# Performance work log

Hardware: AMD Instinct MI355X
Metric: run time of the kernel (lower is better)

## Reference

```python
import jax, jax.numpy as jnp
import numpy as np

N_NODES = 20000
N_EDGES = 320000
IN_F = 256
OUT_F = 64
HEADS = 4
ALPHA = 0.1  # leaky_relu negative slope


def setup_inputs() -> dict:
    key = jax.random.key(0)
    ks = jax.random.split(key, 8)
    return {
        "input1": jax.random.normal(ks[0], (N_NODES, IN_F), jnp.float32),
        "input2": jax.random.normal(ks[1], (N_NODES, IN_F), jnp.float32),
        # per-head params: Ws maps source feats -> target_out, Wt maps target feats -> source_out
        "Ws": jax.random.normal(ks[2], (HEADS, IN_F, OUT_F), jnp.float32) * 0.06,
        "Wt": jax.random.normal(ks[3], (HEADS, IN_F, OUT_F), jnp.float32) * 0.06,
        "a1": jax.random.normal(ks[4], (HEADS, 2 * OUT_F), jnp.float32) * 0.1,
        "a2": jax.random.normal(ks[5], (HEADS, 2 * OUT_F), jnp.float32) * 0.1,
        # COO nonzeros of A_opt [n_target, n_source]
        "tgt_idx": jax.random.randint(ks[6], (N_EDGES,), 0, N_NODES),
        "src_idx": jax.random.randint(ks[7], (N_EDGES,), 0, N_NODES),
    }


def _segment_softmax(scores, seg, num_segments):
    m = jax.lax.stop_gradient(jax.ops.segment_max(scores, seg, num_segments=num_segments))
    w = jnp.exp(scores - m[seg])
    d = jax.ops.segment_sum(w, seg, num_segments=num_segments)
    d = jnp.where(d == 0, 1.0, d)
    return w / d[seg]


def _head(x1, x2, Ws, Wt, a1, a2, src, tgt, n_s, n_t):
    s = x1 @ Ws  # [n_s, OUT_F]  messages source -> target
    t = x2 @ Wt  # [n_t, OUT_F]  messages target -> source
    out = Ws.shape[1]
    # edge score e = leaky_relu(a^T [s_src || t_tgt]); split a to avoid edge-level concat
    e1 = jax.nn.leaky_relu((s @ a1[:out])[src] + (t @ a1[out:])[tgt], ALPHA)
    e2 = jax.nn.leaky_relu((s @ a2[:out])[src] + (t @ a2[out:])[tgt], ALPHA)
    alpha_ts = _segment_softmax(e1, tgt, n_t)  # softmax over sources per target
    alpha_st = _segment_softmax(e2, src, n_s)  # softmax over targets per source
    h_ts = jax.ops.segment_sum(alpha_ts[:, None] * s[src], tgt, num_segments=n_t)
    h_st = jax.ops.segment_sum(alpha_st[:, None] * t[tgt], src, num_segments=n_s)
    return jax.nn.elu(h_st), jax.nn.elu(h_ts)  # concat=True -> ELU per head


def reference(input1, input2, Ws, Wt, a1, a2, tgt_idx, src_idx):
    n_s, n_t = input1.shape[0], input2.shape[0]
    head_fn = jax.vmap(
        lambda W1, W2, v1, v2: _head(input1, input2, W1, W2, v1, v2, src_idx, tgt_idx, n_s, n_t)
    )
    h_st, h_ts = head_fn(Ws, Wt, a1, a2)  # each [H, n, OUT_F]
    h_st = jnp.transpose(h_st, (1, 0, 2)).reshape(n_s, -1)  # concat heads
    h_ts = jnp.transpose(h_ts, (1, 0, 2)).reshape(n_t, -1)
    return h_st, h_ts
```

## Files before the change

### kernel.cpp

```cpp
#include <hip/hip_runtime.h>
#include <math.h>

#define N_NODES 20000
#define N_EDGES 320000
#define IN_F 256
#define OUT_F 64
#define HEADS 4
#define NCOL 256
#define LRELU_ALPHA 0.1f
#define ELL_CAP 64

typedef __attribute__((ext_vector_type(8))) short short8;
typedef __attribute__((ext_vector_type(4))) float floatx4;

__device__ __forceinline__ float lrelu(float x) {
    return x > 0.f ? x : LRELU_ALPHA * x;
}
__device__ __forceinline__ unsigned short f2bf(float f) {
    unsigned int u = __float_as_uint(f);
    u = (u + 0x7FFF + ((u >> 16) & 1)) >> 16;
    return (unsigned short)u;
}
__device__ __forceinline__ float bf2f(unsigned short u) {
    return __uint_as_float(((unsigned int)u) << 16);
}

__global__ __launch_bounds__(256) void prep_w_kernel(
    const float* __restrict__ Ws, const float* __restrict__ Wt,
    unsigned short* __restrict__ Wsb, unsigned short* __restrict__ Wtb,
    int* __restrict__ cnt)
{
    const int gid = blockIdx.x * 256 + threadIdx.x;

    for (int i = gid; i < 2 * N_NODES; i += 16384) cnt[i] = 0;

    const int mat = gid >> 13;
    const int r   = gid & 8191;
    const int kc  = r >> 8;
    const int c   = r & 255;
    const float* W    = mat ? Wt : Ws;
    unsigned short* O = mat ? Wtb : Wsb;
    const int h = c >> 6, j = c & 63;
    const int k0 = kc * 8;
    unsigned short v[8] __attribute__((aligned(16)));
#pragma unroll
    for (int i = 0; i < 8; ++i)
        v[i] = f2bf(W[(size_t)h * (IN_F * OUT_F) + (size_t)(k0 + i) * OUT_F + j]);
    *(uint4*)(O + (size_t)c * IN_F + k0) = *(const uint4*)v;
}

__global__ __launch_bounds__(256) void gemm_mfma_kernel(
    const float* __restrict__ A0, const unsigned short* __restrict__ Wb0,
    const float* __restrict__ A1, const unsigned short* __restrict__ Wb1,
    unsigned short* __restrict__ C0, unsigned short* __restrict__ C1,
    const float* __restrict__ a1, const float* __restrict__ a2,
    float* __restrict__ ss1, float* __restrict__ ss2,
    float* __restrict__ tt1, float* __restrict__ tt2,
    const int* __restrict__ src, const int* __restrict__ tgt,
    int* __restrict__ cnt_t, int* __restrict__ cnt_s,
    int* __restrict__ elist_t, int* __restrict__ elist_s)
{
    const int tid = threadIdx.x;

    {
        const int e = (blockIdx.y * 625 + blockIdx.x) * 256 + tid;
        int sn = src[e], tn = tgt[e];
        int p = atomicAdd(&cnt_t[tn], 1);
        if (p < ELL_CAP) elist_t[tn * ELL_CAP + p] = sn;
        int q = atomicAdd(&cnt_s[sn], 1);
        if (q < ELL_CAP) elist_s[sn * ELL_CAP + q] = tn;
    }

    const float* A           = (blockIdx.y == 0) ? A0 : A1;
    const unsigned short* Wb = (blockIdx.y == 0) ? Wb0 : Wb1;
    unsigned short* C        = (blockIdx.y == 0) ? C0 : C1;

    __shared__ __align__(16) unsigned short Bl[256][40];

    const int lane  = tid & 63;
    const int w     = tid >> 6;
    const int quad  = lane >> 4;
    const int l15   = lane & 15;
    const int mhalf = w & 1, nhalf = w >> 1;
    const int r0    = blockIdx.x * 32;
    const int mrow  = r0 + mhalf * 16 + l15;

    floatx4 acc[8];
#pragma unroll
    for (int t = 0; t < 8; ++t) acc[t] = (floatx4){0.f, 0.f, 0.f, 0.f};

    const float* arow = A + (size_t)mrow * IN_F + quad * 8;

    for (int k0 = 0; k0 < IN_F; k0 += 32) {
#pragma unroll
        for (int p = 0; p < 4; ++p) {
            int idx = p * 256 + tid;
            int n = idx >> 2, kc = idx & 3;
            uint4 v = *(const uint4*)(Wb + (size_t)n * 256 + k0 + kc * 8);
            *(uint4*)&Bl[n][kc * 8] = v;
        }
        __syncthreads();

        float4 av0 = *(const float4*)(arow + k0);
        float4 av1 = *(const float4*)(arow + k0 + 4);
        short8 afrag;
        afrag[0] = (short)f2bf(av0.x); afrag[1] = (short)f2bf(av0.y);
        afrag[2] = (short)f2bf(av0.z); afrag[3] = (short)f2bf(av0.w);
        afrag[4] = (short)f2bf(av1.x); afrag[5] = (short)f2bf(av1.y);
        afrag[6] = (short)f2bf(av1.z); afrag[7] = (short)f2bf(av1.w);

#pragma unroll
        for (int t = 0; t < 8; ++t) {
            int n = (nhalf * 8 + t) * 16 + l15;
            short8 bfrag = *(const short8*)&Bl[n][quad * 8];
            acc[t] = __builtin_amdgcn_mfma_f32_16x16x32_bf16(afrag, bfrag, acc[t], 0, 0, 0);
        }
        __syncthreads();
    }

#pragma unroll
    for (int t = 0; t < 8; ++t) {
        int col = (nhalf * 8 + t) * 16 + l15;
#pragma unroll
        for (int r = 0; r < 4; ++r) {
            int m = r0 + mhalf * 16 + quad * 4 + r;
            C[(size_t)m * NCOL + col] = f2bf(acc[t][r]);
        }
    }

    const int off_aj = (blockIdx.y == 0) ? 0 : 64;
    float* o1 = (blockIdx.y == 0) ? ss1 : tt1;
    float* o2 = (blockIdx.y == 0) ? ss2 : tt2;

    float p1[2][4] = {{0.f,0.f,0.f,0.f},{0.f,0.f,0.f,0.f}};
    float p2[2][4] = {{0.f,0.f,0.f,0.f},{0.f,0.f,0.f,0.f}};
#pragma unroll
    for (int t = 0; t < 8; ++t) {
        int hh = 2 * nhalf + (t >> 2);
        int jj = ((t & 3) * 16) + l15;
        float w1 = a1[hh * 128 + off_aj + jj];
        float w2 = a2[hh * 128 + off_aj + jj];
        int a = t >> 2;
#pragma unroll
        for (int r = 0; r < 4; ++r) {
            p1[a][r] += acc[t][r] * w1;
            p2[a][r] += acc[t][r] * w2;
        }
    }
#pragma unroll
    for (int m = 1; m < 16; m <<= 1) {
#pragma unroll
        for (int a = 0; a < 2; ++a)
#pragma unroll
            for (int r = 0; r < 4; ++r) {
                p1[a][r] += __shfl_xor(p1[a][r], m, 64);
                p2[a][r] += __shfl_xor(p2[a][r], m, 64);
            }
    }
    if (l15 == 0) {
#pragma unroll
        for (int r = 0; r < 4; ++r) {
            int m = r0 + mhalf * 16 + quad * 4 + r;
#pragma unroll
            for (int a = 0; a < 2; ++a) {
                int hh = 2 * nhalf + a;
                o1[m * HEADS + hh] = p1[a][r];
                o2[m * HEADS + hh] = p2[a][r];
            }
        }
    }
}

__global__ __launch_bounds__(256) void agg_kernel(
    const int* __restrict__ cnt_t, const int* __restrict__ elist_t,
    const int* __restrict__ cnt_s, const int* __restrict__ elist_s,
    const float* __restrict__ ss1, const float* __restrict__ ss2,
    const float* __restrict__ tt1, const float* __restrict__ tt2,
    const unsigned short* __restrict__ s_bf, const unsigned short* __restrict__ t_bf,
    float* __restrict__ h_st, float* __restrict__ h_ts)
{
    const int wave = threadIdx.x >> 6;
    const int lane = threadIdx.x & 63;
    const int n    = blockIdx.x * 4 + wave;
    const int dir  = blockIdx.y;
    const int h    = lane >> 4;
    const int coff = lane * 4;

    const int*            cnt   = dir ? cnt_s   : cnt_t;
    const int*            list  = dir ? elist_s : elist_t;
    const unsigned short* table = dir ? t_bf    : s_bf;
    const float*          nsc   = dir ? ss2     : tt1;
    const float*          esc   = dir ? tt2     : ss1;
    float*                outp  = dir ? h_st    : h_ts;

    const float base = nsc[n * HEADS + h];
    int deg = cnt[n];
    if (deg > ELL_CAP) deg = ELL_CAP;
    const int b0 = n * ELL_CAP, b1 = b0 + deg;

    float4 acc = make_float4(0.f, 0.f, 0.f, 0.f);
    float den = 0.f;

    int p = b0;
    for (; p + 3 < b1; p += 4) {
        int m0 = list[p],     m1 = list[p + 1];
        int m2 = list[p + 2], m3 = list[p + 3];
        float e0 = esc[m0 * HEADS + h], e1 = esc[m1 * HEADS + h];
        float e2 = esc[m2 * HEADS + h], e3 = esc[m3 * HEADS + h];
        ushort4 r0 = *(const ushort4*)(table + (size_t)m0 * NCOL + coff);
        ushort4 r1 = *(const ushort4*)(table + (size_t)m1 * NCOL + coff);
        ushort4 r2 = *(const ushort4*)(table + (size_t)m2 * NCOL + coff);
        ushort4 r3 = *(const ushort4*)(table + (size_t)m3 * NCOL + coff);
        float w0 = __expf(lrelu(e0 + base));
        float w1 = __expf(lrelu(e1 + base));
        float w2 = __expf(lrelu(e2 + base));
        float w3 = __expf(lrelu(e3 + base));
        den += (w0 + w1) + (w2 + w3);
        acc.x += (w0 * bf2f(r0.x) + w1 * bf2f(r1.x)) + (w2 * bf2f(r2.x) + w3 * bf2f(r3.x));
        acc.y += (w0 * bf2f(r0.y) + w1 * bf2f(r1.y)) + (w2 * bf2f(r2.y) + w3 * bf2f(r3.y));
        acc.z += (w0 * bf2f(r0.z) + w1 * bf2f(r1.z)) + (w2 * bf2f(r2.z) + w3 * bf2f(r3.z));
        acc.w += (w0 * bf2f(r0.w) + w1 * bf2f(r1.w)) + (w2 * bf2f(r2.w) + w3 * bf2f(r3.w));
    }
    for (; p < b1; ++p) {
        int m0 = list[p];
        float w0 = __expf(lrelu(esc[m0 * HEADS + h] + base));
        ushort4 r0 = *(const ushort4*)(table + (size_t)m0 * NCOL + coff);
        den += w0;
        acc.x += w0 * bf2f(r0.x);
        acc.y += w0 * bf2f(r0.y);
        acc.z += w0 * bf2f(r0.z);
        acc.w += w0 * bf2f(r0.w);
    }

    if (den == 0.f) den = 1.f;
    float inv = 1.f / den;
    float4 r;
    r.x = acc.x * inv; r.y = acc.y * inv; r.z = acc.z * inv; r.w = acc.w * inv;
    r.x = (r.x > 0.f) ? r.x : expm1f(r.x);
    r.y = (r.y > 0.f) ? r.y : expm1f(r.y);
    r.z = (r.z > 0.f) ? r.z : expm1f(r.z);
    r.w = (r.w > 0.f) ? r.w : expm1f(r.w);
    *(float4*)(outp + (size_t)n * NCOL + coff) = r;
}

extern "C" void kernel_launch(void* const* d_in, const int* in_sizes, int n_in,
                              void* d_out, int out_size, void* d_ws, size_t ws_size,
                              hipStream_t stream)
{
    const float* input1 = (const float*)d_in[0];
    const float* input2 = (const float*)d_in[1];
    const float* Ws     = (const float*)d_in[2];
    const float* Wt     = (const float*)d_in[3];
    const float* a1     = (const float*)d_in[4];
    const float* a2     = (const float*)d_in[5];
    const int*   tgt    = (const int*)d_in[6];
    const int*   src    = (const int*)d_in[7];

    float* out  = (float*)d_out;
    float* h_st = out;
    float* h_ts = out + (size_t)N_NODES * NCOL;

    unsigned short* s_bf = (unsigned short*)d_ws;
    unsigned short* t_bf = s_bf + (size_t)N_NODES * NCOL;
    unsigned short* Wsb  = t_bf + (size_t)N_NODES * NCOL;
    unsigned short* Wtb  = Wsb + 256 * 256;
    float* ss1  = (float*)(Wtb + 256 * 256);
    float* ss2  = ss1 + N_NODES * HEADS;
    float* tt1  = ss2 + N_NODES * HEADS;
    float* tt2  = tt1 + N_NODES * HEADS;
    int*   cnt_t = (int*)(tt2 + N_NODES * HEADS);
    int*   cnt_s = cnt_t + N_NODES;
    int*   elist_t = cnt_s + N_NODES;
    int*   elist_s = elist_t + N_NODES * ELL_CAP;

    prep_w_kernel<<<64, 256, 0, stream>>>(Ws, Wt, Wsb, Wtb, cnt_t);

    dim3 ggrid(N_NODES / 32, 2);
    gemm_mfma_kernel<<<ggrid, 256, 0, stream>>>(input1, Wsb, input2, Wtb,
                                                s_bf, t_bf, a1, a2,
                                                ss1, ss2, tt1, tt2,
                                                src, tgt, cnt_t, cnt_s,
                                                elist_t, elist_s);

    dim3 agrid(N_NODES / 4, 2);
    agg_kernel<<<agrid, 256, 0, stream>>>(cnt_t, elist_t, cnt_s, elist_s,
                                          ss1, ss2, tt1, tt2, s_bf, t_bf, h_st, h_ts);
}
```

Before: 203.3 us.

## Split edge scatter into dedicated blocks with batched atomics inside GEMM launch

```diff
diff --git a/kernel.cpp b/kernel.cpp
--- a/kernel.cpp
+++ b/kernel.cpp
@@ -9,6 +9,10 @@
 #define NCOL 256
 #define LRELU_ALPHA 0.1f
 #define ELL_CAP 64
+
+#define SCAT_X 64
+#define SCAT_THREADS (SCAT_X * 2 * 256)
+#define GEMM_BX 625
 
 typedef __attribute__((ext_vector_type(8))) short short8;
 typedef __attribute__((ext_vector_type(4))) float floatx4;
@@ -49,7 +53,19 @@
     *(uint4*)(O + (size_t)c * IN_F + k0) = *(const uint4*)v;
 }
 
-__global__ __launch_bounds__(256) void gemm_mfma_kernel(
+__device__ __forceinline__ void scat_one(
+    int e, const int* __restrict__ src, const int* __restrict__ tgt,
+    int* __restrict__ cnt_t, int* __restrict__ cnt_s,
+    int* __restrict__ elist_t, int* __restrict__ elist_s)
+{
+    int sn = src[e], tn = tgt[e];
+    int p = atomicAdd(&cnt_t[tn], 1);
+    if (p < ELL_CAP) elist_t[tn * ELL_CAP + p] = sn;
+    int q = atomicAdd(&cnt_s[sn], 1);
+    if (q < ELL_CAP) elist_s[sn * ELL_CAP + q] = tn;
+}
+
+__global__ __launch_bounds__(256) void gemm_hybrid_kernel(
     const float* __restrict__ A0, const unsigned short* __restrict__ Wb0,
     const float* __restrict__ A1, const unsigned short* __restrict__ Wb1,
     unsigned short* __restrict__ C0, unsigned short* __restrict__ C1,
@@ -62,15 +78,38 @@
 {
     const int tid = threadIdx.x;
 
-    {
-        const int e = (blockIdx.y * 625 + blockIdx.x) * 256 + tid;
-        int sn = src[e], tn = tgt[e];
-        int p = atomicAdd(&cnt_t[tn], 1);
-        if (p < ELL_CAP) elist_t[tn * ELL_CAP + p] = sn;
-        int q = atomicAdd(&cnt_s[sn], 1);
-        if (q < ELL_CAP) elist_s[sn * ELL_CAP + q] = tn;
-    }
-
+    if (blockIdx.x < SCAT_X) {
+        const int base = (blockIdx.y * SCAT_X + blockIdx.x) * 256 + tid;
+        int e = base;
+        for (; e + 3 * SCAT_THREADS < N_EDGES; e += 4 * SCAT_THREADS) {
+            int e0 = e, e1 = e + SCAT_THREADS, e2 = e + 2 * SCAT_THREADS, e3 = e + 3 * SCAT_THREADS;
+            int s0 = src[e0], t0 = tgt[e0];
+            int s1 = src[e1], t1 = tgt[e1];
+            int s2 = src[e2], t2 = tgt[e2];
+            int s3 = src[e3], t3 = tgt[e3];
+            int p0 = atomicAdd(&cnt_t[t0], 1);
+            int q0 = atomicAdd(&cnt_s[s0], 1);
+            int p1 = atomicAdd(&cnt_t[t1], 1);
+            int q1 = atomicAdd(&cnt_s[s1], 1);
+            int p2 = atomicAdd(&cnt_t[t2], 1);
+            int q2 = atomicAdd(&cnt_s[s2], 1);
+            int p3 = atomicAdd(&cnt_t[t3], 1);
+            int q3 = atomicAdd(&cnt_s[s3], 1);
+            if (p0 < ELL_CAP) elist_t[t0 * ELL_CAP + p0] = s0;
+            if (q0 < ELL_CAP) elist_s[s0 * ELL_CAP + q0] = t0;
+            if (p1 < ELL_CAP) elist_t[t1 * ELL_CAP + p1] = s1;
+            if (q1 < ELL_CAP) elist_s[s1 * ELL_CAP + q1] = t1;
+            if (p2 < ELL_CAP) elist_t[t2 * ELL_CAP + p2] = s2;
+            if (q2 < ELL_CAP) elist_s[s2 * ELL_CAP + q2] = t2;
+            if (p3 < ELL_CAP) elist_t[t3 * ELL_CAP + p3] = s3;
+            if (q3 < ELL_CAP) elist_s[s3 * ELL_CAP + q3] = t3;
+        }
+        for (; e < N_EDGES; e += SCAT_THREADS)
+            scat_one(e, src, tgt, cnt_t, cnt_s, elist_t, elist_s);
+        return;
+    }
+
+    const int bx = blockIdx.x - SCAT_X;
     const float* A           = (blockIdx.y == 0) ? A0 : A1;
     const unsigned short* Wb = (blockIdx.y == 0) ? Wb0 : Wb1;
     unsigned short* C        = (blockIdx.y == 0) ? C0 : C1;
@@ -82,7 +121,7 @@
     const int quad  = lane >> 4;
     const int l15   = lane & 15;
     const int mhalf = w & 1, nhalf = w >> 1;
-    const int r0    = blockIdx.x * 32;
+    const int r0    = bx * 32;
     const int mrow  = r0 + mhalf * 16 + l15;
 
     floatx4 acc[8];
@@ -275,12 +314,12 @@
 
     prep_w_kernel<<<64, 256, 0, stream>>>(Ws, Wt, Wsb, Wtb, cnt_t);
 
-    dim3 ggrid(N_NODES / 32, 2);
-    gemm_mfma_kernel<<<ggrid, 256, 0, stream>>>(input1, Wsb, input2, Wtb,
-                                                s_bf, t_bf, a1, a2,
-                                                ss1, ss2, tt1, tt2,
-                                                src, tgt, cnt_t, cnt_s,
-                                                elist_t, elist_s);
+    dim3 ggrid(SCAT_X + GEMM_BX, 2);
+    gemm_hybrid_kernel<<<ggrid, 256, 0, stream>>>(input1, Wsb, input2, Wtb,
+                                                  s_bf, t_bf, a1, a2,
+                                                  ss1, ss2, tt1, tt2,
+                                                  src, tgt, cnt_t, cnt_s,
+                                                  elist_t, elist_s);
 
     dim3 agrid(N_NODES / 4, 2);
     agg_kernel<<<agrid, 256, 0, stream>>>(cnt_t, elist_t, cnt_s, elist_s,
```

Result: faster. 190.9 us (-6.1%).
